# Performance work log

Measured on AMD Instinct MI355X. Metric: run time of the kernel, lower is better.

## Reference

```python
import jax, jax.numpy as jnp
import numpy as np

B, D, H = 32768, 1024, 8
LN_EPS = 1e-5


def setup_inputs() -> dict:
    key = jax.random.key(0)
    ks = jax.random.split(key, 12)
    w = lambda k, shape: (jax.random.normal(k, shape, dtype=jnp.float32) * 0.02)
    inp = {
        "graph_embedding": jax.random.normal(ks[0], (B, D), dtype=jnp.float32),
        "smiles_embedding": jax.random.normal(ks[1], (B, D), dtype=jnp.float32),
        "num_heads": H,
        # cross_attn_graph_to_smiles params (torch MHA: in_proj [3D,D] split q/k/v, out_proj [D,D])
        "Wq_gs": w(ks[2], (D, D)), "Wk_gs": w(ks[3], (D, D)), "Wv_gs": w(ks[4], (D, D)),
        "bq_gs": jnp.zeros((D,), jnp.float32), "bk_gs": jnp.zeros((D,), jnp.float32), "bv_gs": jnp.zeros((D,), jnp.float32),
        "Wo_gs": w(ks[5], (D, D)), "bo_gs": jnp.zeros((D,), jnp.float32),
        # cross_attn_smiles_to_graph params
        "Wq_sg": w(ks[6], (D, D)), "Wk_sg": w(ks[7], (D, D)), "Wv_sg": w(ks[8], (D, D)),
        "bq_sg": jnp.zeros((D,), jnp.float32), "bk_sg": jnp.zeros((D,), jnp.float32), "bv_sg": jnp.zeros((D,), jnp.float32),
        "Wo_sg": w(ks[9], (D, D)), "bo_sg": jnp.zeros((D,), jnp.float32),
        # LayerNorms
        "ln_g_gamma": jnp.ones((D,), jnp.float32), "ln_g_beta": jnp.zeros((D,), jnp.float32),
        "ln_s_gamma": jnp.ones((D,), jnp.float32), "ln_s_beta": jnp.zeros((D,), jnp.float32),
        # Gate: Linear(2D -> D) then sigmoid
        "Wg": w(ks[10], (D, 2 * D)), "bg": jnp.zeros((D,), jnp.float32),
    }
    return inp


def _layernorm(x, gamma, beta):
    mu = jnp.mean(x, axis=-1, keepdims=True)
    var = jnp.mean(jnp.square(x - mu), axis=-1, keepdims=True)
    return (x - mu) * jax.lax.rsqrt(var + LN_EPS) * gamma + beta


def _mha_len1(kv, Wv, bv, Wo, bo):
    # seq_len=1 cross-attention: softmax over a single key is identically 1,
    # so output == out_proj(v_proj(kv)). q/k projections contribute nothing
    # (and have exactly zero gradient), matching torch's math.
    v = kv @ Wv.T + bv
    return v @ Wo.T + bo


def reference(graph_embedding, smiles_embedding, num_heads,
              Wq_gs, Wk_gs, Wv_gs, bq_gs, bk_gs, bv_gs, Wo_gs, bo_gs,
              Wq_sg, Wk_sg, Wv_sg, bq_sg, bk_sg, bv_sg, Wo_sg, bo_sg,
              ln_g_gamma, ln_g_beta, ln_s_gamma, ln_s_beta, Wg, bg):
    # dropout p=0 / eval mode -> identity
    attn_g2s = _mha_len1(smiles_embedding, Wv_gs, bv_gs, Wo_gs, bo_gs)  # graph queries smiles
    attn_s2g = _mha_len1(graph_embedding, Wv_sg, bv_sg, Wo_sg, bo_sg)   # smiles queries graph
    fused_graph = _layernorm(graph_embedding + attn_g2s, ln_g_gamma, ln_g_beta)
    fused_smiles = _layernorm(smiles_embedding + attn_s2g, ln_s_gamma, ln_s_beta)
    gate_in = jnp.concatenate([fused_graph, fused_smiles], axis=1)  # [B, 2D]
    gate_weight = jax.nn.sigmoid(gate_in @ Wg.T + bg)               # [B, D]
    fused_feature = gate_weight * fused_graph + (1.0 - gate_weight) * fused_smiles
    return fused_feature, gate_weight
```

## Files before the change

### kernel.cpp

```cpp
#include <hip/hip_runtime.h>

#define BROWS 32768
#define DDIM 1024

typedef __bf16 bf16x8v __attribute__((ext_vector_type(8)));
typedef float f32x4v __attribute__((ext_vector_type(4)));

__device__ __forceinline__ float bf2f(unsigned short u) {
  union { unsigned int i; float f; } w; w.i = ((unsigned int)u) << 16; return w.f;
}
__device__ __forceinline__ unsigned short f2bf(float f) {
  union { float f; unsigned int i; } w; w.f = f;
  w.i += 0x7fffu + ((w.i >> 16) & 1u);
  return (unsigned short)(w.i >> 16);
}

__device__ __forceinline__ void gl_lds16(const void* g, void* l) {
  __builtin_amdgcn_global_load_lds((const __attribute__((address_space(1))) void*)g,
                                   (__attribute__((address_space(3))) void*)l, 16, 0, 0);
}

__device__ __forceinline__ int xcd_swz(int bid, int nwg) {
  return (bid & 7) * (nwg >> 3) + (bid >> 3);
}

__device__ __forceinline__ int swzc(int row, int col) {
  return (col & ~63) | ((col & 63) ^ ((row & 7) << 3));
}

__global__ __launch_bounds__(256) void cvt_x(const float* __restrict__ g,
                                             const float* __restrict__ s,
                                             unsigned short* __restrict__ xg,
                                             unsigned short* __restrict__ xs) {
  const size_t N = (size_t)BROWS * DDIM;
  size_t i = ((size_t)blockIdx.x * 256 + threadIdx.x) * 4;
  const float* src = (i < N) ? g : s;
  unsigned short* dst = (i < N) ? xg : xs;
  size_t off = (i < N) ? i : i - N;
  int row = (int)(off >> 10), col = (int)(off & 1023);
  float4 v = *(const float4*)&src[off];
  union { uint2 q; unsigned short h[4]; } u;
  u.h[0] = f2bf(v.x); u.h[1] = f2bf(v.y); u.h[2] = f2bf(v.z); u.h[3] = f2bf(v.w);
  *(uint2*)&dst[(size_t)row * DDIM + swzc(row, col)] = u.q;
}

__global__ __launch_bounds__(256) void cvt_wg(const float* __restrict__ s,
                                              unsigned short* __restrict__ d) {
  int i = (blockIdx.x * 256 + threadIdx.x) * 4;
  int row = i >> 11, col = i & 2047;
  float4 v = *(const float4*)&s[i];
  union { uint2 q; unsigned short h[4]; } u;
  u.h[0] = f2bf(v.x); u.h[1] = f2bf(v.y); u.h[2] = f2bf(v.z); u.h[3] = f2bf(v.w);
  *(uint2*)&d[(size_t)row * 2048 + swzc(row, col)] = u.q;
}

__global__ __launch_bounds__(256) void bias_combine(
    const float* __restrict__ Wo_gs, const float* __restrict__ bv_gs,
    const float* __restrict__ bo_gs,
    const float* __restrict__ Wo_sg, const float* __restrict__ bv_sg,
    const float* __restrict__ bo_sg,
    float* __restrict__ bc_gs, float* __restrict__ bc_sg) {
  int gid = blockIdx.x * 256 + threadIdx.x;
  int pair = gid >> 10, j = gid & 1023;
  const float* Wo = pair ? Wo_sg : Wo_gs;
  const float* bv = pair ? bv_sg : bv_gs;
  const float* bo = pair ? bo_sg : bo_gs;
  float s = 0.f;
  for (int k = 0; k < DDIM; k += 4) {
    float4 w = *(const float4*)&Wo[(size_t)j * DDIM + k];
    float4 b = *(const float4*)&bv[k];
    s += w.x * b.x + w.y * b.y + w.z * b.z + w.w * b.w;
  }
  float* bc = pair ? bc_sg : bc_gs;
  bc[j] = s + bo[j];
}

__device__ __forceinline__ void stage_f32_32(const float* __restrict__ src, int ldk,
                                             int row0, int k0, unsigned short* lds, int tid) {
  const int sr = tid >> 2, sc = (tid & 3) * 8;
#pragma unroll
  for (int h = 0; h < 2; ++h) {
    const float* g = &src[(size_t)(row0 + h * 64 + sr) * ldk + k0 + sc];
    float4 va = ((const float4*)g)[0];
    float4 vb = ((const float4*)g)[1];
    union { uint4 q; unsigned short hh[8]; } u;
    u.hh[0] = f2bf(va.x); u.hh[1] = f2bf(va.y); u.hh[2] = f2bf(va.z); u.hh[3] = f2bf(va.w);
    u.hh[4] = f2bf(vb.x); u.hh[5] = f2bf(vb.y); u.hh[6] = f2bf(vb.z); u.hh[7] = f2bf(vb.w);
    *(uint4*)&lds[(h * 64 + sr) * 32 + sc] = u.q;
  }
}

__device__ __forceinline__ void mfma_tile32(const unsigned short* As, const unsigned short* Bs,
                                            int ab, int bb, f32x4v acc[4][4]) {
  const bf16x8v* Av = reinterpret_cast<const bf16x8v*>(As);
  const bf16x8v* Bv = reinterpret_cast<const bf16x8v*>(Bs);
  bf16x8v af[4], bfr[4];
#pragma unroll
  for (int m = 0; m < 4; ++m) af[m] = Av[ab + m * 64];
#pragma unroll
  for (int n = 0; n < 4; ++n) bfr[n] = Bv[bb + n * 64];
#pragma unroll
  for (int m = 0; m < 4; ++m)
#pragma unroll
    for (int n = 0; n < 4; ++n)
      acc[m][n] = __builtin_amdgcn_mfma_f32_16x16x32_bf16(af[m], bfr[n], acc[m][n], 0, 0, 0);
}

__global__ __launch_bounds__(256) void combine_kernel(
    const float* __restrict__ Wo_gs, const float* __restrict__ Wv_gs,
    const float* __restrict__ Wo_sg, const float* __restrict__ Wv_sg,
    unsigned short* __restrict__ Wc_gs, unsigned short* __restrict__ Wc_sg) {
  const int pair = blockIdx.y;
  const float* Wo = pair ? Wo_sg : Wo_gs;
  const float* Wv = pair ? Wv_sg : Wv_gs;
  unsigned short* Wc = pair ? Wc_sg : Wc_gs;
  const int mt = blockIdx.x >> 3, nt = blockIdx.x & 7;
  const int row0 = mt * 128, col0 = nt * 128;

  __shared__ __align__(16) unsigned short As[128 * 32];
  __shared__ __align__(16) unsigned short Bt[128 * 32];

  const int tid = threadIdx.x;
  const int lane = tid & 63, wave = tid >> 6;
  const int wr = wave >> 1, wc = wave & 1;
  const int lr = lane & 15, lk = lane >> 4;

  f32x4v acc[4][4] = {};
  const int ab = (wr * 64 + lr) * 4 + lk;
  const int bb = (wc * 64 + lr) * 4 + lk;

  for (int tt = 0; tt < 32; ++tt) {
    const int t0 = tt * 32;
    __syncthreads();
    stage_f32_32(Wo, DDIM, row0, t0, As, tid);
#pragma unroll
    for (int h = 0; h < 2; ++h) {
      int chunk = h * 256 + tid;
      int t = chunk >> 4;
      int c8 = (chunk & 15) * 8;
      const float* g = &Wv[(size_t)(t0 + t) * DDIM + col0 + c8];
      float4 va = ((const float4*)g)[0];
      float4 vb = ((const float4*)g)[1];
      float vv[8] = {va.x, va.y, va.z, va.w, vb.x, vb.y, vb.z, vb.w};
#pragma unroll
      for (int e = 0; e < 8; ++e) Bt[(c8 + e) * 32 + t] = f2bf(vv[e]);
    }
    __syncthreads();
    mfma_tile32(As, Bt, ab, bb, acc);
  }

#pragma unroll
  for (int n = 0; n < 4; ++n) {
    int col = col0 + wc * 64 + n * 16 + lr;
#pragma unroll
    for (int m = 0; m < 4; ++m) {
      int rbase = row0 + wr * 64 + m * 16 + lk * 4;
#pragma unroll
      for (int r = 0; r < 4; ++r)
        Wc[(size_t)(rbase + r) * DDIM + swzc(rbase + r, col)] = f2bf(acc[m][n][r]);
    }
  }
}


__global__ __launch_bounds__(512, 2) void gemm_branch8(
    const unsigned short* __restrict__ Xs_b, const unsigned short* __restrict__ Xg_b,
    const unsigned short* __restrict__ Wc_gs, const unsigned short* __restrict__ Wc_sg,
    const float* __restrict__ bc_gs, const float* __restrict__ bc_sg,
    unsigned short* __restrict__ Zg, unsigned short* __restrict__ Zs) {
  const int pair = blockIdx.y;
  const unsigned short* X = pair ? Xg_b : Xs_b;
  const unsigned short* residb = pair ? Xs_b : Xg_b;
  const unsigned short* Wc = pair ? Wc_sg : Wc_gs;
  const float* bc = pair ? bc_sg : bc_gs;
  unsigned short* Z = pair ? Zs : Zg;

  const int bid = xcd_swz(blockIdx.x, 1024);
  const int mt = bid >> 2, nt = bid & 3;
  const int row0 = mt * 128, col0 = nt * 256;
  const int NT = 16;

  __shared__ __align__(16) unsigned short As[4][128 * 64];
  __shared__ __align__(16) unsigned short Bs[2][256 * 64];

  const int tid = threadIdx.x;
  const int lane = tid & 63, wave = tid >> 6;
  const int wm = wave >> 2, wn = wave & 3;
  const int lr = lane & 15, lk = lane >> 4;

  f32x4v acc[4][4] = {};

  auto stageB = [&](int kt, int jj) {
    int idx = jj * 512 + tid, row = idx >> 3, ch = idx & 7;
    gl_lds16(&Wc[(size_t)(col0 + row) * DDIM + kt * 64 + ch * 8], &Bs[kt & 1][idx * 8]);
  };
  auto stageA = [&](int kt, int jj) {
    int idx = jj * 512 + tid, row = idx >> 3, ch = idx & 7;
    gl_lds16(&X[(size_t)(row0 + row) * DDIM + kt * 64 + ch * 8], &As[kt & 3][idx * 8]);
  };

  stageB(0, 0); stageB(0, 1); stageB(0, 2); stageB(0, 3);
  stageA(0, 0); stageA(0, 1);
  stageA(1, 0); stageA(1, 1);
  stageA(2, 0); stageA(2, 1);

  for (int kt = 0; kt < NT; ++kt) {
    if (kt == 0)          asm volatile("s_waitcnt vmcnt(4)" ::: "memory");
    else if (kt < NT - 3) asm volatile("s_waitcnt vmcnt(2)" ::: "memory");
    else                  asm volatile("s_waitcnt vmcnt(0)" ::: "memory");
    asm volatile("s_barrier" ::: "memory");
    if (kt + 1 < NT) { stageB(kt + 1, 0); stageB(kt + 1, 1);
                       stageB(kt + 1, 2); stageB(kt + 1, 3); }
    if (kt + 3 < NT) { stageA(kt + 3, 0); stageA(kt + 3, 1); }

    const unsigned short* Ak = As[kt & 3];
    const unsigned short* Bk = Bs[kt & 1];
    bf16x8v bv[4][2], av[4][2];
#pragma unroll
    for (int n = 0; n < 4; ++n)
#pragma unroll
      for (int s = 0; s < 2; ++s) {
        int row = wn * 64 + n * 16 + lr;
        bv[n][s] = *(const bf16x8v*)&Bk[row * 64 + (((s * 4 + lk) ^ (row & 7)) * 8)];
      }
#pragma unroll
    for (int m = 0; m < 4; ++m)
#pragma unroll
      for (int s = 0; s < 2; ++s) {
        int row = wm * 64 + m * 16 + lr;
        av[m][s] = *(const bf16x8v*)&Ak[row * 64 + (((s * 4 + lk) ^ (row & 7)) * 8)];
      }
    __builtin_amdgcn_s_setprio(1);
#pragma unroll
    for (int s = 0; s < 2; ++s)
#pragma unroll
      for (int m = 0; m < 4; ++m)
#pragma unroll
        for (int n = 0; n < 4; ++n)
          acc[m][n] = __builtin_amdgcn_mfma_f32_16x16x32_bf16(av[m][s], bv[n][s],
                                                              acc[m][n], 0, 0, 0);
    __builtin_amdgcn_s_setprio(0);
  }

#pragma unroll
  for (int n = 0; n < 4; ++n) {
    int col = col0 + wn * 64 + n * 16 + lr;
    float bcv = bc[col];
#pragma unroll
    for (int m = 0; m < 4; ++m) {
      int rb = row0 + wm * 64 + m * 16 + lk * 4;
#pragma unroll
      for (int r = 0; r < 4; ++r) {
        int row = rb + r;
        size_t idx = (size_t)row * DDIM + swzc(row, col);
        Z[idx] = f2bf(acc[m][n][r] + bcv + bf2f(residb[idx]));
      }
    }
  }
}

__global__ __launch_bounds__(512, 2) void gemm_gate8(
    const unsigned short* __restrict__ fg, const unsigned short* __restrict__ fs,
    const unsigned short* __restrict__ WgB, const float* __restrict__ bg,
    float* __restrict__ out0, float* __restrict__ out1) {
  const int bid = xcd_swz(blockIdx.x, 1024);
  const int mt = bid >> 2, nt = bid & 3;
  const int row0 = mt * 128, col0 = nt * 256;
  const int NT = 32;

  __shared__ __align__(16) unsigned short As[4][128 * 64];
  __shared__ __align__(16) unsigned short Bs[2][256 * 64];

  const int tid = threadIdx.x;
  const int lane = tid & 63, wave = tid >> 6;
  const int wm = wave >> 2, wn = wave & 3;
  const int lr = lane & 15, lk = lane >> 4;

  f32x4v acc[4][4] = {};

  auto stageB = [&](int kt, int jj) {
    int idx = jj * 512 + tid, row = idx >> 3, ch = idx & 7;
    gl_lds16(&WgB[(size_t)(col0 + row) * 2048 + kt * 64 + ch * 8], &Bs[kt & 1][idx * 8]);
  };
  auto stageA = [&](int kt, int jj) {
    const unsigned short* asrc = (kt < 16) ? fg : fs;
    int ak0 = (kt & 15) * 64;
    int idx = jj * 512 + tid, row = idx >> 3, ch = idx & 7;
    gl_lds16(&asrc[(size_t)(row0 + row) * DDIM + ak0 + ch * 8], &As[kt & 3][idx * 8]);
  };

  stageB(0, 0); stageB(0, 1); stageB(0, 2); stageB(0, 3);
  stageA(0, 0); stageA(0, 1);
  stageA(1, 0); stageA(1, 1);
  stageA(2, 0); stageA(2, 1);

  for (int kt = 0; kt < NT; ++kt) {
    if (kt == 0)          asm volatile("s_waitcnt vmcnt(4)" ::: "memory");
    else if (kt < NT - 3) asm volatile("s_waitcnt vmcnt(2)" ::: "memory");
    else                  asm volatile("s_waitcnt vmcnt(0)" ::: "memory");
    asm volatile("s_barrier" ::: "memory");
    if (kt + 1 < NT) { stageB(kt + 1, 0); stageB(kt + 1, 1);
                       stageB(kt + 1, 2); stageB(kt + 1, 3); }
    if (kt + 3 < NT) { stageA(kt + 3, 0); stageA(kt + 3, 1); }

    const unsigned short* Ak = As[kt & 3];
    const unsigned short* Bk = Bs[kt & 1];
    bf16x8v bv[4][2], av[4][2];
#pragma unroll
    for (int n = 0; n < 4; ++n)
#pragma unroll
      for (int s = 0; s < 2; ++s) {
        int row = wn * 64 + n * 16 + lr;
        bv[n][s] = *(const bf16x8v*)&Bk[row * 64 + (((s * 4 + lk) ^ (row & 7)) * 8)];
      }
#pragma unroll
    for (int m = 0; m < 4; ++m)
#pragma unroll
      for (int s = 0; s < 2; ++s) {
        int row = wm * 64 + m * 16 + lr;
        av[m][s] = *(const bf16x8v*)&Ak[row * 64 + (((s * 4 + lk) ^ (row & 7)) * 8)];
      }
    __builtin_amdgcn_s_setprio(1);
#pragma unroll
    for (int s = 0; s < 2; ++s)
#pragma unroll
      for (int m = 0; m < 4; ++m)
#pragma unroll
        for (int n = 0; n < 4; ++n)
          acc[m][n] = __builtin_amdgcn_mfma_f32_16x16x32_bf16(av[m][s], bv[n][s],
                                                              acc[m][n], 0, 0, 0);
    __builtin_amdgcn_s_setprio(0);
  }

#pragma unroll
  for (int n = 0; n < 4; ++n) {
    int col = col0 + wn * 64 + n * 16 + lr;
    float bgv = bg[col];
#pragma unroll
    for (int m = 0; m < 4; ++m) {
      int rb = row0 + wm * 64 + m * 16 + lk * 4;
#pragma unroll
      for (int r = 0; r < 4; ++r) {
        int row = rb + r;
        size_t sidx = (size_t)row * DDIM + swzc(row, col);
        size_t tidx = (size_t)row * DDIM + col;
        float g = 1.f / (1.f + __expf(-(acc[m][n][r] + bgv)));
        float a = bf2f(fg[sidx]), b = bf2f(fs[sidx]);
        out0[tidx] = g * a + (1.f - g) * b;
        out1[tidx] = g;
      }
    }
  }
}

__global__ __launch_bounds__(256) void ln_kernel(
    unsigned short* __restrict__ Z,
    const float* __restrict__ gam_g, const float* __restrict__ bet_g,
    const float* __restrict__ gam_s, const float* __restrict__ bet_s) {
  int row = blockIdx.x * 4 + (threadIdx.x >> 6);
  int lane = threadIdx.x & 63;
  const float* gam = (row < BROWS) ? gam_g : gam_s;
  const float* bet = (row < BROWS) ? bet_g : bet_s;
  unsigned short* zr = Z + (size_t)row * DDIM;

  uint4 v0 = *(const uint4*)(zr + lane * 8);
  uint4 v1 = *(const uint4*)(zr + 512 + lane * 8);
  const unsigned short* u0 = (const unsigned short*)&v0;
  const unsigned short* u1 = (const unsigned short*)&v1;
  float x[16];
  float s = 0.f, sq = 0.f;
#pragma unroll
  for (int e = 0; e < 8; ++e) { x[e] = bf2f(u0[e]); x[8 + e] = bf2f(u1[e]); }
#pragma unroll
  for (int i = 0; i < 16; ++i) { s += x[i]; sq += x[i] * x[i]; }
#pragma unroll
  for (int o = 32; o; o >>= 1) { s += __shfl_xor(s, o); sq += __shfl_xor(sq, o); }
  float mu = s * (1.f / 1024.f);
  float var = sq * (1.f / 1024.f) - mu * mu;
  float rstd = rsqrtf(var + 1e-5f);

  int lane2 = (lane & ~7) | ((lane & 7) ^ (row & 7));
  float4 g0 = *(const float4*)(gam + lane2 * 8);
  float4 g1 = *(const float4*)(gam + lane2 * 8 + 4);
  float4 g2 = *(const float4*)(gam + 512 + lane2 * 8);
  float4 g3 = *(const float4*)(gam + 512 + lane2 * 8 + 4);
  float4 b0 = *(const float4*)(bet + lane2 * 8);
  float4 b1 = *(const float4*)(bet + lane2 * 8 + 4);
  float4 b2 = *(const float4*)(bet + 512 + lane2 * 8);
  float4 b3 = *(const float4*)(bet + 512 + lane2 * 8 + 4);
  float gg[16] = {g0.x,g0.y,g0.z,g0.w,g1.x,g1.y,g1.z,g1.w,
                  g2.x,g2.y,g2.z,g2.w,g3.x,g3.y,g3.z,g3.w};
  float bb[16] = {b0.x,b0.y,b0.z,b0.w,b1.x,b1.y,b1.z,b1.w,
                  b2.x,b2.y,b2.z,b2.w,b3.x,b3.y,b3.z,b3.w};

  union { uint4 q; unsigned short h[8]; } o0, o1;
#pragma unroll
  for (int e = 0; e < 8; ++e) {
    o0.h[e] = f2bf((x[e] - mu) * rstd * gg[e] + bb[e]);
    o1.h[e] = f2bf((x[8 + e] - mu) * rstd * gg[8 + e] + bb[8 + e]);
  }
  *(uint4*)(zr + lane * 8) = o0.q;
  *(uint4*)(zr + 512 + lane * 8) = o1.q;
}

__global__ __launch_bounds__(256) void gemm_gate_f32(
    const unsigned short* __restrict__ fg, const unsigned short* __restrict__ fs,
    const float* __restrict__ Wg, const float* __restrict__ bg,
    float* __restrict__ out0, float* __restrict__ out1) {
  const int bid = xcd_swz(blockIdx.x, 2048);
  const int mt = bid >> 3, nt = bid & 7;
  const int row0 = mt * 128, col0 = nt * 128;

  __shared__ __align__(16) unsigned short As[128 * 64];
  __shared__ __align__(16) unsigned short Bsh[128 * 64];

  const int tid = threadIdx.x;
  const int lane = tid & 63, wave = tid >> 6;
  const int wr = wave >> 1, wc = wave & 1;
  const int lr = lane & 15, lk = lane >> 4;

  f32x4v acc[4][4] = {};

  for (int kt = 0; kt < 32; ++kt) {
    const unsigned short* Asrc = (kt < 16) ? fg : fs;
    const int k0 = (kt & 15) * 64;
    const int kw = kt * 64;
    __syncthreads();
#pragma unroll
    for (int h = 0; h < 4; ++h) {
      int row = h * 32 + (tid >> 3);
      gl_lds16(&Asrc[(size_t)(row0 + row) * DDIM + k0 + (tid & 7) * 8], &As[h * 2048 + tid * 8]);
    }
#pragma unroll
    for (int h = 0; h < 4; ++h) {
      int row = h * 32 + (tid >> 3), c16 = tid & 7;
      const float* gsrc = &Wg[(size_t)(col0 + row) * 2048 + kw + c16 * 8];
      float4 va = ((const float4*)gsrc)[0];
      float4 vb = ((const float4*)gsrc)[1];
      union { uint4 q; unsigned short hh[8]; } u;
      u.hh[0] = f2bf(va.x); u.hh[1] = f2bf(va.y); u.hh[2] = f2bf(va.z); u.hh[3] = f2bf(va.w);
      u.hh[4] = f2bf(vb.x); u.hh[5] = f2bf(vb.y); u.hh[6] = f2bf(vb.z); u.hh[7] = f2bf(vb.w);
      *(uint4*)&Bsh[(row * 8 + (c16 ^ (row & 7))) * 8] = u.q;
    }
    __syncthreads();
    const bf16x8v* Av = reinterpret_cast<const bf16x8v*>(As);
    const bf16x8v* Bv = reinterpret_cast<const bf16x8v*>(Bsh);
    const int xr = lr & 7;
#pragma unroll
    for (int s = 0; s < 2; ++s) {
      const int u = (s * 4 + lk) ^ xr;
      bf16x8v af[4], bfr[4];
#pragma unroll
      for (int m = 0; m < 4; ++m) af[m] = Av[(wr * 64 + m * 16 + lr) * 8 + u];
#pragma unroll
      for (int n = 0; n < 4; ++n) bfr[n] = Bv[(wc * 64 + n * 16 + lr) * 8 + u];
#pragma unroll
      for (int m = 0; m < 4; ++m)
#pragma unroll
        for (int n = 0; n < 4; ++n)
          acc[m][n] = __builtin_amdgcn_mfma_f32_16x16x32_bf16(af[m], bfr[n], acc[m][n], 0, 0, 0);
    }
  }

#pragma unroll
  for (int n = 0; n < 4; ++n) {
    int col = col0 + wc * 64 + n * 16 + lr;
    float bgv = bg[col];
#pragma unroll
    for (int m = 0; m < 4; ++m) {
      int rbase = row0 + wr * 64 + m * 16 + lk * 4;
#pragma unroll
      for (int r = 0; r < 4; ++r) {
        int row = rbase + r;
        size_t sidx = (size_t)row * DDIM + swzc(row, col);
        size_t tidx = (size_t)row * DDIM + col;
        float g = 1.f / (1.f + __expf(-(acc[m][n][r] + bgv)));
        float a = bf2f(fg[sidx]), b = bf2f(fs[sidx]);
        out0[tidx] = g * a + (1.f - g) * b;
        out1[tidx] = g;
      }
    }
  }
}

extern "C" void kernel_launch(void* const* d_in, const int* in_sizes, int n_in,
                              void* d_out, int out_size, void* d_ws, size_t ws_size,
                              hipStream_t stream) {
  const float* graph  = (const float*)d_in[0];
  const float* smiles = (const float*)d_in[1];
  const float* Wv_gs  = (const float*)d_in[5];
  const float* bv_gs  = (const float*)d_in[8];
  const float* Wo_gs  = (const float*)d_in[9];
  const float* bo_gs  = (const float*)d_in[10];
  const float* Wv_sg  = (const float*)d_in[13];
  const float* bv_sg  = (const float*)d_in[16];
  const float* Wo_sg  = (const float*)d_in[17];
  const float* bo_sg  = (const float*)d_in[18];
  const float* ln_gg  = (const float*)d_in[19];
  const float* ln_gb  = (const float*)d_in[20];
  const float* ln_sg  = (const float*)d_in[21];
  const float* ln_sb  = (const float*)d_in[22];
  const float* Wg     = (const float*)d_in[23];
  const float* bg     = (const float*)d_in[24];

  char* ob = (char*)d_out;
  unsigned short* Xg_b  = (unsigned short*)ob;
  unsigned short* Xs_b  = (unsigned short*)(ob + (64u << 20));
  unsigned short* Wc_gs = (unsigned short*)(ob + (128u << 20));
  unsigned short* Wc_sg = (unsigned short*)(ob + (130u << 20));
  float* bc_gs = (float*)(ob + (132u << 20));
  float* bc_sg = (float*)(ob + (132u << 20) + 4096);

  unsigned short* Zg = (unsigned short*)d_ws;
  unsigned short* Zs = Zg + (size_t)BROWS * DDIM;
  const bool fast = ws_size >= ((size_t)132 << 20);
  unsigned short* WgB = (unsigned short*)((char*)d_ws + ((size_t)128 << 20));

  float* out0 = (float*)d_out;
  float* out1 = out0 + (size_t)BROWS * DDIM;

  cvt_x<<<dim3(65536), dim3(256), 0, stream>>>(graph, smiles, Xg_b, Xs_b);
  bias_combine<<<dim3(8), dim3(256), 0, stream>>>(Wo_gs, bv_gs, bo_gs, Wo_sg, bv_sg, bo_sg,
                                                  bc_gs, bc_sg);
  combine_kernel<<<dim3(64, 2), dim3(256), 0, stream>>>(Wo_gs, Wv_gs, Wo_sg, Wv_sg,
                                                        Wc_gs, Wc_sg);
  if (fast) cvt_wg<<<dim3(2048), dim3(256), 0, stream>>>(Wg, WgB);
  gemm_branch8<<<dim3(1024, 2), dim3(512), 0, stream>>>(Xs_b, Xg_b, Wc_gs, Wc_sg,
                                                        bc_gs, bc_sg, Zg, Zs);
  ln_kernel<<<dim3(16384), dim3(256), 0, stream>>>(Zg, ln_gg, ln_gb, ln_sg, ln_sb);
  if (fast)
    gemm_gate8<<<dim3(1024), dim3(512), 0, stream>>>(Zg, Zs, WgB, bg, out0, out1);
  else
    gemm_gate_f32<<<dim3(2048), dim3(256), 0, stream>>>(Zg, Zs, Wg, bg, out0, out1);
}
```

Measured before the change: 765.5 us.

## Shrink GEMM tiles to 128x128 with 256 threads and shallower A pipeline

Both bf16 MFMA GEMMs (branch and gate) move from a 128x256 tile with 512 threads to a 128x128 tile with 256 threads (4 waves), which doubles the grid. The A-operand prefetch ring drops from 4 to 3 stages with a lookahead of 2, and the vmcnt waits are adjusted to match. Smaller LDS use and blocks are meant to raise occupancy and balance load across CUs. In exchange, each block reuses less data per byte loaded and the weight matrix is read more times in total.

```diff
diff --git a/kernel.cpp b/kernel.cpp
--- a/kernel.cpp
+++ b/kernel.cpp
@@ -163,7 +163,7 @@
 }
 
 
-__global__ __launch_bounds__(512, 2) void gemm_branch8(
+__global__ __launch_bounds__(256, 2) void gemm_branch8(
     const unsigned short* __restrict__ Xs_b, const unsigned short* __restrict__ Xg_b,
     const unsigned short* __restrict__ Wc_gs, const unsigned short* __restrict__ Wc_sg,
     const float* __restrict__ bc_gs, const float* __restrict__ bc_sg,
@@ -175,45 +175,49 @@
   const float* bc = pair ? bc_sg : bc_gs;
   unsigned short* Z = pair ? Zs : Zg;
 
-  const int bid = xcd_swz(blockIdx.x, 1024);
-  const int mt = bid >> 2, nt = bid & 3;
-  const int row0 = mt * 128, col0 = nt * 256;
+  const int bid = xcd_swz(blockIdx.x, 2048);
+  const int mt = bid >> 3, nt = bid & 7;
+  const int row0 = mt * 128, col0 = nt * 128;
   const int NT = 16;
 
-  __shared__ __align__(16) unsigned short As[4][128 * 64];
-  __shared__ __align__(16) unsigned short Bs[2][256 * 64];
+  __shared__ __align__(16) unsigned short As[3][128 * 64];
+  __shared__ __align__(16) unsigned short Bs[2][128 * 64];
 
   const int tid = threadIdx.x;
   const int lane = tid & 63, wave = tid >> 6;
-  const int wm = wave >> 2, wn = wave & 3;
+  const int wm = wave >> 1, wn = wave & 1;
   const int lr = lane & 15, lk = lane >> 4;
 
   f32x4v acc[4][4] = {};
 
-  auto stageB = [&](int kt, int jj) {
-    int idx = jj * 512 + tid, row = idx >> 3, ch = idx & 7;
-    gl_lds16(&Wc[(size_t)(col0 + row) * DDIM + kt * 64 + ch * 8], &Bs[kt & 1][idx * 8]);
+  auto stageB = [&](int kt) {
+#pragma unroll
+    for (int r = 0; r < 4; ++r) {
+      int idx = r * 2048 + tid * 8;
+      int row = idx >> 6, ch = (tid & 7) * 8;
+      gl_lds16(&Wc[(size_t)(col0 + row) * DDIM + kt * 64 + ch], &Bs[kt & 1][idx]);
+    }
   };
-  auto stageA = [&](int kt, int jj) {
-    int idx = jj * 512 + tid, row = idx >> 3, ch = idx & 7;
-    gl_lds16(&X[(size_t)(row0 + row) * DDIM + kt * 64 + ch * 8], &As[kt & 3][idx * 8]);
+  auto stageA = [&](int kt) {
+    int slot = kt - (kt / 3) * 3;
+#pragma unroll
+    for (int r = 0; r < 4; ++r) {
+      int idx = r * 2048 + tid * 8;
+      int row = idx >> 6, ch = (tid & 7) * 8;
+      gl_lds16(&X[(size_t)(row0 + row) * DDIM + kt * 64 + ch], &As[slot][idx]);
+    }
   };
 
-  stageB(0, 0); stageB(0, 1); stageB(0, 2); stageB(0, 3);
-  stageA(0, 0); stageA(0, 1);
-  stageA(1, 0); stageA(1, 1);
-  stageA(2, 0); stageA(2, 1);
+  stageB(0); stageA(0); stageA(1);
 
   for (int kt = 0; kt < NT; ++kt) {
-    if (kt == 0)          asm volatile("s_waitcnt vmcnt(4)" ::: "memory");
-    else if (kt < NT - 3) asm volatile("s_waitcnt vmcnt(2)" ::: "memory");
-    else                  asm volatile("s_waitcnt vmcnt(0)" ::: "memory");
+    if (kt < NT - 1) asm volatile("s_waitcnt vmcnt(4)" ::: "memory");
+    else             asm volatile("s_waitcnt vmcnt(0)" ::: "memory");
     asm volatile("s_barrier" ::: "memory");
-    if (kt + 1 < NT) { stageB(kt + 1, 0); stageB(kt + 1, 1);
-                       stageB(kt + 1, 2); stageB(kt + 1, 3); }
-    if (kt + 3 < NT) { stageA(kt + 3, 0); stageA(kt + 3, 1); }
-
-    const unsigned short* Ak = As[kt & 3];
+    if (kt + 1 < NT) stageB(kt + 1);
+    if (kt + 2 < NT) stageA(kt + 2);
+
+    const unsigned short* Ak = As[kt - (kt / 3) * 3];
     const unsigned short* Bk = Bs[kt & 1];
     bf16x8v bv[4][2], av[4][2];
 #pragma unroll
@@ -259,51 +263,55 @@
   }
 }
 
-__global__ __launch_bounds__(512, 2) void gemm_gate8(
+__global__ __launch_bounds__(256, 2) void gemm_gate8(
     const unsigned short* __restrict__ fg, const unsigned short* __restrict__ fs,
     const unsigned short* __restrict__ WgB, const float* __restrict__ bg,
     float* __restrict__ out0, float* __restrict__ out1) {
-  const int bid = xcd_swz(blockIdx.x, 1024);
-  const int mt = bid >> 2, nt = bid & 3;
-  const int row0 = mt * 128, col0 = nt * 256;
+  const int bid = xcd_swz(blockIdx.x, 2048);
+  const int mt = bid >> 3, nt = bid & 7;
+  const int row0 = mt * 128, col0 = nt * 128;
   const int NT = 32;
 
-  __shared__ __align__(16) unsigned short As[4][128 * 64];
-  __shared__ __align__(16) unsigned short Bs[2][256 * 64];
+  __shared__ __align__(16) unsigned short As[3][128 * 64];
+  __shared__ __align__(16) unsigned short Bs[2][128 * 64];
 
   const int tid = threadIdx.x;
   const int lane = tid & 63, wave = tid >> 6;
-  const int wm = wave >> 2, wn = wave & 3;
+  const int wm = wave >> 1, wn = wave & 1;
   const int lr = lane & 15, lk = lane >> 4;
 
   f32x4v acc[4][4] = {};
 
-  auto stageB = [&](int kt, int jj) {
-    int idx = jj * 512 + tid, row = idx >> 3, ch = idx & 7;
-    gl_lds16(&WgB[(size_t)(col0 + row) * 2048 + kt * 64 + ch * 8], &Bs[kt & 1][idx * 8]);
+  auto stageB = [&](int kt) {
+#pragma unroll
+    for (int r = 0; r < 4; ++r) {
+      int idx = r * 2048 + tid * 8;
+      int row = idx >> 6, ch = (tid & 7) * 8;
+      gl_lds16(&WgB[(size_t)(col0 + row) * 2048 + kt * 64 + ch], &Bs[kt & 1][idx]);
+    }
   };
-  auto stageA = [&](int kt, int jj) {
+  auto stageA = [&](int kt) {
     const unsigned short* asrc = (kt < 16) ? fg : fs;
     int ak0 = (kt & 15) * 64;
-    int idx = jj * 512 + tid, row = idx >> 3, ch = idx & 7;
-    gl_lds16(&asrc[(size_t)(row0 + row) * DDIM + ak0 + ch * 8], &As[kt & 3][idx * 8]);
+    int slot = kt - (kt / 3) * 3;
+#pragma unroll
+    for (int r = 0; r < 4; ++r) {
+      int idx = r * 2048 + tid * 8;
+      int row = idx >> 6, ch = (tid & 7) * 8;
+      gl_lds16(&asrc[(size_t)(row0 + row) * DDIM + ak0 + ch], &As[slot][idx]);
+    }
   };
 
-  stageB(0, 0); stageB(0, 1); stageB(0, 2); stageB(0, 3);
-  stageA(0, 0); stageA(0, 1);
-  stageA(1, 0); stageA(1, 1);
-  stageA(2, 0); stageA(2, 1);
+  stageB(0); stageA(0); stageA(1);
 
   for (int kt = 0; kt < NT; ++kt) {
-    if (kt == 0)          asm volatile("s_waitcnt vmcnt(4)" ::: "memory");
-    else if (kt < NT - 3) asm volatile("s_waitcnt vmcnt(2)" ::: "memory");
-    else                  asm volatile("s_waitcnt vmcnt(0)" ::: "memory");
+    if (kt < NT - 1) asm volatile("s_waitcnt vmcnt(4)" ::: "memory");
+    else             asm volatile("s_waitcnt vmcnt(0)" ::: "memory");
     asm volatile("s_barrier" ::: "memory");
-    if (kt + 1 < NT) { stageB(kt + 1, 0); stageB(kt + 1, 1);
-                       stageB(kt + 1, 2); stageB(kt + 1, 3); }
-    if (kt + 3 < NT) { stageA(kt + 3, 0); stageA(kt + 3, 1); }
-
-    const unsigned short* Ak = As[kt & 3];
+    if (kt + 1 < NT) stageB(kt + 1);
+    if (kt + 2 < NT) stageA(kt + 2);
+
+    const unsigned short* Ak = As[kt - (kt / 3) * 3];
     const unsigned short* Bk = Bs[kt & 1];
     bf16x8v bv[4][2], av[4][2];
 #pragma unroll
@@ -525,11 +533,11 @@
   combine_kernel<<<dim3(64, 2), dim3(256), 0, stream>>>(Wo_gs, Wv_gs, Wo_sg, Wv_sg,
                                                         Wc_gs, Wc_sg);
   if (fast) cvt_wg<<<dim3(2048), dim3(256), 0, stream>>>(Wg, WgB);
-  gemm_branch8<<<dim3(1024, 2), dim3(512), 0, stream>>>(Xs_b, Xg_b, Wc_gs, Wc_sg,
+  gemm_branch8<<<dim3(2048, 2), dim3(256), 0, stream>>>(Xs_b, Xg_b, Wc_gs, Wc_sg,
                                                         bc_gs, bc_sg, Zg, Zs);
   ln_kernel<<<dim3(16384), dim3(256), 0, stream>>>(Zg, ln_gg, ln_gb, ln_sg, ln_sb);
   if (fast)
-    gemm_gate8<<<dim3(1024), dim3(512), 0, stream>>>(Zg, Zs, WgB, bg, out0, out1);
+    gemm_gate8<<<dim3(2048), dim3(256), 0, stream>>>(Zg, Zs, WgB, bg, out0, out1);
   else
     gemm_gate_f32<<<dim3(2048), dim3(256), 0, stream>>>(Zg, Zs, Wg, bg, out0, out1);
 }
```

Measured after the change: 706.3 us (median of 2 runs). 7.7% less time.
